# Kernel optimization log

Measured on AMD Instinct MI355X. Metric: run time of the kernel, lower is better.

The kernel has to match this reference:

```python
import jax, jax.numpy as jnp
import numpy as np
from jax import lax

N, C, A, K, D = 2, 256, 3, 20, 256  # batch, channels, anchors, topk person cells, rn_fc_dim
BOX = 4
SIZES = [(80, 128), (40, 64), (20, 32), (10, 16)]
DN = ('NCHW', 'OIHW', 'NCHW')


def _conv(x, w, b):
    return lax.conv_general_dilated(x, w, (1, 1), 'SAME', dimension_numbers=DN) + b[None, :, None, None]


def setup_inputs() -> dict:
    key = jax.random.key(0)
    ks = iter(jax.random.split(key, 40))
    d = {}
    for i, (h, w) in enumerate(SIZES):
        d['feat%d' % i] = jax.random.normal(next(ks), (N, C, h, w), jnp.float32)
    def wfn(shape, s=0.05):
        return jax.random.normal(next(ks), shape, jnp.float32) * s
    d['pc1_w'] = wfn((C, C, 3, 3)); d['pc1_b'] = jnp.zeros((C,), jnp.float32)
    d['pc2_w'] = wfn((C, C, 3, 3)); d['pc2_b'] = jnp.zeros((C,), jnp.float32)
    d['oc1_w'] = wfn((C, C, 3, 3)); d['oc1_b'] = jnp.zeros((C,), jnp.float32)
    d['oc2_w'] = wfn((C, C, 3, 3)); d['oc2_b'] = jnp.zeros((C,), jnp.float32)
    # relation-net FCs: first takes concat(object, person) -> 2C in
    d['rn1_w'] = wfn((D, 2 * C)); d['rn1_b'] = jnp.zeros((D,), jnp.float32)
    d['rn2_w'] = wfn((D, D)); d['rn2_b'] = jnp.zeros((D,), jnp.float32)
    # heads
    d['pl_w'] = wfn((A, C, 1, 1), 0.01); d['pl_b'] = jnp.zeros((A,), jnp.float32)
    d['pd_w'] = wfn((A * BOX, C, 1, 1), 0.01); d['pd_b'] = jnp.zeros((A * BOX,), jnp.float32)
    d['ol_w'] = wfn((A, D), 0.01); d['ol_b'] = jnp.zeros((A,), jnp.float32)
    d['od_w'] = wfn((A * BOX, C, 1, 1), 0.01); d['od_b'] = jnp.zeros((A * BOX,), jnp.float32)
    return d


def _find_top_cells(hidden, logits, topk):
    hid_l, sc_l = [], []
    for h_map, lg in zip(hidden, logits):
        n, c, H, W = h_map.shape
        cell_scores = jnp.max(lg, axis=1).reshape(n, -1)          # (N, HW)
        ts, tc = lax.top_k(cell_scores, topk)                      # (N, K)
        hv = h_map.reshape(n, c, -1)                               # (N, C, HW)
        hid_l.append(jnp.take_along_axis(hv, tc[:, None, :], axis=2))  # (N, C, K)
        sc_l.append(ts)
    scores = jnp.concatenate(sc_l, axis=1)                         # (N, L*K)
    hid = jnp.concatenate(hid_l, axis=2)                           # (N, C, L*K)
    _, keep = lax.top_k(scores, topk)
    return jnp.take_along_axis(hid, keep[:, None, :], axis=2)      # (N, C, K)


def _forward(feats, pc1_w, pc1_b, pc2_w, pc2_b, oc1_w, oc1_b, oc2_w, oc2_b,
             rn1_w, rn1_b, rn2_w, rn2_b, pl_w, pl_b, pd_w, pd_b, ol_w, ol_b, od_w, od_b):
    # person branch
    p_hid, p_log, p_del = [], [], []
    for x in feats:
        x = jax.nn.relu(_conv(x, pc1_w, pc1_b))
        x = jax.nn.relu(_conv(x, pc2_w, pc2_b))
        p_hid.append(x)
        p_log.append(_conv(x, pl_w, pl_b))
        p_del.append(_conv(x, pd_w, pd_b))
    topk_person = _find_top_cells(p_hid, p_log, K)                 # (N, C, K)
    pf = topk_person.transpose(0, 2, 1)                            # (N, K, C)
    # object branch: fc1(concat(o, p)) == o @ Wo.T + p @ Wp.T + b (concat order: object first)
    Wo, Wp = rn1_w[:, :C], rn1_w[:, C:]
    p_proj = jnp.einsum('nkc,dc->nkd', pf, Wp) + rn1_b             # (N, K, D)
    o_log, o_del = [], []
    for x in feats:
        n, _, H, W = x.shape
        y = jax.nn.relu(_conv(x, oc1_w, oc1_b))
        y = jax.nn.relu(_conv(y, oc2_w, oc2_b))
        o_del.append(_conv(y, od_w, od_b))
        yf = y.reshape(n, C, H * W).transpose(0, 2, 1)             # (N, HW, C)
        o_proj = jnp.einsum('nsc,dc->nsd', yf, Wo)                 # (N, HW, D)
        h = jax.nn.relu(o_proj[:, :, None, :] + p_proj[:, None, :, :])  # (N, HW, K, D)
        h = h.sum(axis=2)                                          # (N, HW, D)
        h = jax.nn.relu(jnp.einsum('nsd,ed->nse', h, rn2_w) + rn2_b)
        ol = jnp.einsum('nsd,ad->nsa', h, ol_w) + ol_b             # (N, HW, A)
        o_log.append(ol.transpose(0, 2, 1).reshape(n, A, H, W))
    return tuple(p_log) + tuple(p_del) + tuple(o_log) + tuple(o_del)


def reference(feat0, feat1, feat2, feat3, pc1_w, pc1_b, pc2_w, pc2_b, oc1_w, oc1_b, oc2_w, oc2_b,
              rn1_w, rn1_b, rn2_w, rn2_b, pl_w, pl_b, pd_w, pd_b, ol_w, ol_b, od_w, od_b):
    return _forward([feat0, feat1, feat2, feat3], pc1_w, pc1_b, pc2_w, pc2_b, oc1_w, oc1_b,
                    oc2_w, oc2_b, rn1_w, rn1_b, rn2_w, rn2_b, pl_w, pl_b, pd_w, pd_b,
                    ol_w, ol_b, od_w, od_b)
```

## Files before the change

### kernel.cpp

```cpp
#include <hip/hip_runtime.h>
#include <cstdint>
#include <cstddef>

typedef __bf16 bf16x8 __attribute__((ext_vector_type(8)));
typedef float  f32x16 __attribute__((ext_vector_type(16)));

union U16 { bf16x8 v; uint4 q; };
union U8  { __bf16 h[4]; unsigned long long u; };

__device__ __forceinline__ int lvl256(int bx) {
    return (bx < 40) ? 0 : (bx < 50) ? 1 : (bx < 53) ? 2 : 3;
}
__device__ __forceinline__ int tbase256(int lv) {
    return (lv == 0) ? 0 : (lv == 1) ? 40 : (lv == 2) ? 50 : 53;
}
__device__ __forceinline__ size_t loffE(int lv) {
    return (lv == 0) ? 0 : (lv == 1) ? 5242880 : (lv == 2) ? 6553600 : 6881280;
}
__device__ __forceinline__ size_t plog_off(int lv) {
    return (lv == 0) ? 0 : (lv == 1) ? 61440 : (lv == 2) ? 76800 : 80640;
}
__device__ __forceinline__ size_t pdel_off(int lv) {
    return (lv == 0) ? 81600 : (lv == 1) ? 327360 : (lv == 2) ? 388800 : 404160;
}
__device__ __forceinline__ size_t olog_off(int lv) {
    return (lv == 0) ? 408000 : (lv == 1) ? 469440 : (lv == 2) ? 484800 : 488640;
}
__device__ __forceinline__ size_t odel_off(int lv) {
    return (lv == 0) ? 489600 : (lv == 1) ? 735360 : (lv == 2) ? 796800 : 812160;
}
__device__ __forceinline__ int soff_l(int lv) {
    return (lv == 0) ? 0 : (lv == 1) ? 20480 : (lv == 2) ? 25600 : 26880;
}

__global__ __launch_bounds__(256) void prep_wtap2_k(
    const float* w0, const float* w1, const float* w2, const float* w3,
    __bf16* d0, __bf16* d1, __bf16* d2, __bf16* d3)
{
    int t = blockIdx.x % 9, which = blockIdx.x / 9;
    int co = blockIdx.y, ci = threadIdx.x;
    const float* src = (which == 0) ? w0 : (which == 1) ? w1 : (which == 2) ? w2 : w3;
    __bf16* dst = (which == 0) ? d0 : (which == 1) ? d1 : (which == 2) ? d2 : d3;
    dst[((size_t)(t * 16 + (ci >> 4)) * 256 + co) * 16 + (ci & 15)] =
        (__bf16)src[(size_t)(co * 256 + ci) * 9 + t];
}

__global__ __launch_bounds__(256) void prep_rel_k(
    const float* __restrict__ rn1w, const float* __restrict__ rn2w,
    float* __restrict__ WpT, __bf16* __restrict__ Wo16, __bf16* __restrict__ rn216,
    unsigned* __restrict__ zrow32)
{
    int d = blockIdx.x, c = threadIdx.x;
    WpT[c * 256 + d] = rn1w[(size_t)d * 512 + 256 + c];
    Wo16[((c >> 4) * 256 + d) * 16 + (c & 15)] = (__bf16)rn1w[(size_t)d * 512 + c];
    rn216[((c >> 4) * 256 + d) * 16 + (c & 15)] = (__bf16)rn2w[(size_t)d * 256 + c];
    if (d == 0 && c < 256) zrow32[c] = 0u;
}

__global__ __launch_bounds__(256) void feat2x16_k(
    const float* f0, const float* f1, const float* f2, const float* f3,
    __bf16* __restrict__ x16)
{
    int bx = blockIdx.x, n = blockIdx.y, z = blockIdx.z;
    int lv = lvl256(bx);
    int HW = 10240 >> (2 * lv);
    int p = (bx - tbase256(lv)) * 256 + threadIdx.x;
    if (p >= HW) return;
    const float* f = (lv == 0) ? f0 : (lv == 1) ? f1 : (lv == 2) ? f2 : f3;
    int ch = z >> 1, u = z & 1;
    const float* src = f + (size_t)n * 256 * HW + (size_t)(ch * 16 + u * 8) * HW + p;
    U16 v;
#pragma unroll
    for (int j = 0; j < 8; ++j) v.v[j] = (__bf16)src[(size_t)j * HW];
    *(uint4*)&x16[loffE(lv) + (size_t)n * HW * 256 + (((size_t)ch * HW + p) << 4) + (u << 3)] = v.q;
}

__global__ __launch_bounds__(256) void conv3x3_v3(
    const __bf16* __restrict__ in16,
    const __bf16* __restrict__ wt0, const __bf16* __restrict__ wt1,
    const float* __restrict__ b0p, const float* __restrict__ b1p,
    const __bf16* __restrict__ zrow,
    __bf16* __restrict__ out0, __bf16* __restrict__ out1)
{
    const int tid = threadIdx.x;
    const int zz = blockIdx.z;
    const int n = zz & 1, br = zz >> 1;
    const __bf16* wt = br ? wt1 : wt0;
    const float* bias = br ? b1p : b0p;
    __bf16* outp = br ? out1 : out0;

    const int bx = blockIdx.x;
    const int lv = lvl256(bx);
    const int lg2W = 7 - lv;
    const int W = 1 << lg2W, H = 80 >> lv;
    const int HW = 10240 >> (2 * lv);
    const size_t ioff = loffE(lv) + (size_t)n * HW * 256;
    const __bf16* inb = in16 + ioff;

    const int tile = bx - tbase256(lv);
    const int sp0 = tile << 8;
    const int npix = min(256, HW - sp0);

    const int w = tid >> 6, l64 = tid & 63;
    const int lane = l64 & 31, half = l64 >> 5;
    const int pix0 = (w << 6) + lane, pix1 = pix0 + 32;
    const int cobase = blockIdx.y << 6;

    int boff0[9], boff1[9];
    {
        const int y0 = sp0 >> lg2W;
        const int py0 = pix0 >> lg2W, px0 = pix0 & (W - 1);
        const int py1 = pix1 >> lg2W, px1 = pix1 & (W - 1);
#pragma unroll
        for (int dy = 0; dy < 3; ++dy)
#pragma unroll
            for (int dx = 0; dx < 3; ++dx) {
                int t = dy * 3 + dx;
                int gy0 = y0 + py0 + dy - 1, gx0 = px0 + dx - 1;
                boff0[t] = ((unsigned)gy0 < (unsigned)H && (unsigned)gx0 < (unsigned)W)
                           ? (((gy0 << lg2W) + gx0) * 32 + half * 16) : -1;
                int gy1 = y0 + py1 + dy - 1, gx1 = px1 + dx - 1;
                boff1[t] = ((unsigned)gy1 < (unsigned)H && (unsigned)gx1 < (unsigned)W)
                           ? (((gy1 << lg2W) + gx1) * 32 + half * 16) : -1;
            }
    }
    const __bf16* zp = zrow + (half << 3);

    f32x16 acc00 = {}, acc01 = {}, acc10 = {}, acc11 = {};

    for (int c16 = 0; c16 < 16; ++c16) {
        const char* curB = (const char*)inb + (size_t)c16 * HW * 32;
        const char* curA = (const char*)wt + ((size_t)c16 * 256 + cobase) * 32
                           + lane * 32 + half * 16;
#pragma unroll
        for (int t = 0; t < 9; ++t) {
            const char* ab = curA + (size_t)t * 131072;
            bf16x8 a0 = *(const bf16x8*)ab;
            bf16x8 a1 = *(const bf16x8*)(ab + 1024);
            const __bf16* q0 = (boff0[t] >= 0) ? (const __bf16*)(curB + boff0[t]) : zp;
            const __bf16* q1 = (boff1[t] >= 0) ? (const __bf16*)(curB + boff1[t]) : zp;
            bf16x8 b0 = *(const bf16x8*)q0;
            bf16x8 b1 = *(const bf16x8*)q1;
            acc00 = __builtin_amdgcn_mfma_f32_32x32x16_bf16(a0, b0, acc00, 0, 0, 0);
            acc01 = __builtin_amdgcn_mfma_f32_32x32x16_bf16(a0, b1, acc01, 0, 0, 0);
            acc10 = __builtin_amdgcn_mfma_f32_32x32x16_bf16(a1, b0, acc10, 0, 0, 0);
            acc11 = __builtin_amdgcn_mfma_f32_32x32x16_bf16(a1, b1, acc11, 0, 0, 0);
        }
    }
    const int pixg0 = sp0 + pix0, pixg1 = sp0 + pix1;
    const bool ok0 = (pix0 < npix), ok1 = (pix1 < npix);
#pragma unroll
    for (int b = 0; b < 2; ++b) {
        const f32x16& A0 = b ? acc10 : acc00;
        const f32x16& A1 = b ? acc11 : acc01;
#pragma unroll
        for (int q = 0; q < 4; ++q) {
            int co0 = cobase + b * 32 + q * 8 + half * 4;
            float4 bq = *(const float4*)&bias[co0];
            U8 v0, v1;
            v0.h[0] = (__bf16)fmaxf(A0[q * 4 + 0] + bq.x, 0.f);
            v0.h[1] = (__bf16)fmaxf(A0[q * 4 + 1] + bq.y, 0.f);
            v0.h[2] = (__bf16)fmaxf(A0[q * 4 + 2] + bq.z, 0.f);
            v0.h[3] = (__bf16)fmaxf(A0[q * 4 + 3] + bq.w, 0.f);
            v1.h[0] = (__bf16)fmaxf(A1[q * 4 + 0] + bq.x, 0.f);
            v1.h[1] = (__bf16)fmaxf(A1[q * 4 + 1] + bq.y, 0.f);
            v1.h[2] = (__bf16)fmaxf(A1[q * 4 + 2] + bq.z, 0.f);
            v1.h[3] = (__bf16)fmaxf(A1[q * 4 + 3] + bq.w, 0.f);
            size_t base = ioff + (((size_t)(co0 >> 4) * HW) << 4) + (co0 & 15);
            if (ok0) *(unsigned long long*)&outp[base + ((size_t)pixg0 << 4)] = v0.u;
            if (ok1) *(unsigned long long*)&outp[base + ((size_t)pixg1 << 4)] = v1.u;
        }
    }
}

__global__ __launch_bounds__(256) void p_heads_v2(
    const __bf16* __restrict__ h16, const float* __restrict__ plw,
    const float* __restrict__ plb, const float* __restrict__ pdw,
    const float* __restrict__ pdb, float* __restrict__ out,
    float* __restrict__ scores)
{
    int bx = blockIdx.x, n = blockIdx.y;
    int lv = lvl256(bx);
    int HW = 10240 >> (2 * lv);
    int p = (bx - tbase256(lv)) * 256 + threadIdx.x;
    if (p >= HW) return;
    size_t ioff = loffE(lv) + (size_t)n * HW * 256;
    float acc[15];
#pragma unroll
    for (int a = 0; a < 15; ++a) acc[a] = 0.f;
    for (int ch = 0; ch < 16; ++ch) {
        size_t base = ioff + (((size_t)ch * HW + p) << 4);
        bf16x8 v0 = *(const bf16x8*)&h16[base];
        bf16x8 v1 = *(const bf16x8*)&h16[base + 8];
#pragma unroll
        for (int j = 0; j < 16; ++j) {
            float vv = (j < 8) ? (float)v0[j] : (float)v1[j - 8];
            int c = ch * 16 + j;
#pragma unroll
            for (int a = 0; a < 3; ++a)  acc[a]     = fmaf(plw[a * 256 + c], vv, acc[a]);
#pragma unroll
            for (int a = 0; a < 12; ++a) acc[3 + a] = fmaf(pdw[a * 256 + c], vv, acc[3 + a]);
        }
    }
    float sc = -INFINITY;
#pragma unroll
    for (int a = 0; a < 3; ++a) {
        float lg = acc[a] + plb[a];
        out[plog_off(lv) + ((size_t)n * 3 + a) * HW + p] = lg;
        sc = fmaxf(sc, lg);
    }
    scores[soff_l(lv) + (size_t)n * HW + p] = sc;
#pragma unroll
    for (int a = 0; a < 12; ++a)
        out[pdel_off(lv) + ((size_t)n * 12 + a) * HW + p] = acc[3 + a] + pdb[a];
}

__global__ __launch_bounds__(256) void o_del_v2(
    const __bf16* __restrict__ h16, const float* __restrict__ odw,
    const float* __restrict__ odb, float* __restrict__ out)
{
    int bx = blockIdx.x, n = blockIdx.y;
    int lv = lvl256(bx);
    int HW = 10240 >> (2 * lv);
    int p = (bx - tbase256(lv)) * 256 + threadIdx.x;
    if (p >= HW) return;
    size_t ioff = loffE(lv) + (size_t)n * HW * 256;
    float acc[12];
#pragma unroll
    for (int a = 0; a < 12; ++a) acc[a] = 0.f;
    for (int ch = 0; ch < 16; ++ch) {
        size_t base = ioff + (((size_t)ch * HW + p) << 4);
        bf16x8 v0 = *(const bf16x8*)&h16[base];
        bf16x8 v1 = *(const bf16x8*)&h16[base + 8];
#pragma unroll
        for (int j = 0; j < 16; ++j) {
            float vv = (j < 8) ? (float)v0[j] : (float)v1[j - 8];
            int c = ch * 16 + j;
#pragma unroll
            for (int a = 0; a < 12; ++a) acc[a] = fmaf(odw[a * 256 + c], vv, acc[a]);
        }
    }
#pragma unroll
    for (int a = 0; a < 12; ++a)
        out[odel_off(lv) + ((size_t)n * 12 + a) * HW + p] = acc[a] + odb[a];
}

__global__ __launch_bounds__(256) void topk_level_k(
    const float* __restrict__ scores, float* __restrict__ lv_sc,
    int* __restrict__ lv_ix)
{
    int l = blockIdx.x, n = blockIdx.y;
    int HW = 10240 >> (2 * l);
    int so = soff_l(l);
    __shared__ float sc[10240];
    __shared__ float rv[256];
    __shared__ int   ri[256];
    int tid = threadIdx.x;
    for (int i = tid; i < HW; i += 256) sc[i] = scores[so + (size_t)n * HW + i];
    __syncthreads();
    for (int r = 0; r < 20; ++r) {
        float bv = -INFINITY; int bi = 0x7fffffff;
        for (int i = tid; i < HW; i += 256) {
            float v = sc[i];
            if (v > bv || (v == bv && i < bi)) { bv = v; bi = i; }
        }
        rv[tid] = bv; ri[tid] = bi;
        __syncthreads();
        for (int off = 128; off > 0; off >>= 1) {
            if (tid < off) {
                float v2 = rv[tid + off]; int i2 = ri[tid + off];
                if (v2 > rv[tid] || (v2 == rv[tid] && i2 < ri[tid])) {
                    rv[tid] = v2; ri[tid] = i2;
                }
            }
            __syncthreads();
        }
        if (tid == 0) {
            int idx = (n * 4 + l) * 20 + r;
            lv_sc[idx] = rv[0];
            lv_ix[idx] = ri[0];
            sc[ri[0]] = -INFINITY;
        }
        __syncthreads();
    }
}

__global__ __launch_bounds__(256) void select_gather_v2(
    const float* __restrict__ lv_sc, const int* __restrict__ lv_ix,
    const __bf16* __restrict__ h16, float* __restrict__ pf)
{
    int n = blockIdx.x;
    __shared__ float gsc[80];
    __shared__ int   gcell[80];
    __shared__ int   selL[20], selC[20];
    __shared__ float rv[256];
    __shared__ int   ri[256];
    int tid = threadIdx.x;
    if (tid < 80) {
        gsc[tid] = lv_sc[n * 80 + tid];
        gcell[tid] = lv_ix[n * 80 + tid];
    }
    __syncthreads();
    for (int r = 0; r < 20; ++r) {
        float bv = -INFINITY; int bi = 0x7fffffff;
        if (tid < 80) { bv = gsc[tid]; bi = tid; }
        rv[tid] = bv; ri[tid] = bi;
        __syncthreads();
        for (int off = 128; off > 0; off >>= 1) {
            if (tid < off) {
                float v2 = rv[tid + off]; int i2 = ri[tid + off];
                if (v2 > rv[tid] || (v2 == rv[tid] && i2 < ri[tid])) {
                    rv[tid] = v2; ri[tid] = i2;
                }
            }
            __syncthreads();
        }
        if (tid == 0) {
            int j = ri[0];
            selL[r] = j / 20;
            selC[r] = gcell[j];
            gsc[j] = -INFINITY;
        }
        __syncthreads();
    }
    for (int t = tid; t < 20 * 256; t += 256) {
        int k = t >> 8, c = t & 255;
        int l = selL[k], cell = selC[k];
        int HW = 10240 >> (2 * l);
        pf[((size_t)n * 20 + k) * 256 + c] =
            (float)h16[loffE(l) + (size_t)n * HW * 256 +
                       (((size_t)(c >> 4) * HW + cell) << 4) + (c & 15)];
    }
}

__global__ __launch_bounds__(256) void pproj_k(
    const float* __restrict__ pf, const float* __restrict__ WpT,
    const float* __restrict__ rn1b, float* __restrict__ pp)
{
    int nk = blockIdx.x;
    int t = threadIdx.x;
    __shared__ float f[256];
    f[t] = pf[(size_t)nk * 256 + t];
    __syncthreads();
    float acc = rn1b[t];
    for (int c = 0; c < 256; ++c) acc = fmaf(f[c], WpT[c * 256 + t], acc);
    pp[(size_t)nk * 256 + t] = acc;
}

__global__ __launch_bounds__(256) void orel_k(
    const __bf16* __restrict__ H16o, const __bf16* __restrict__ Wo16,
    const __bf16* __restrict__ rn216, const float* __restrict__ pp,
    const float* __restrict__ rn2b, const float* __restrict__ olw,
    const float* __restrict__ olb, float* __restrict__ out)
{
    __shared__ __bf16 hb[16 * 64 * 24];
    __shared__ __bf16 pp16[5120];
    const int tid = threadIdx.x;
    const int n = blockIdx.y;
    int bx = blockIdx.x;
    int lv = (bx < 160) ? 0 : (bx < 200) ? 1 : (bx < 210) ? 2 : 3;
    int tb = (lv == 0) ? 0 : (lv == 1) ? 160 : (lv == 2) ? 200 : 210;
    int HW = 10240 >> (2 * lv);
    size_t yoff = loffE(lv) + (size_t)n * HW * 256;
    int p0 = (bx - tb) << 6;
    int npix = min(64, HW - p0);

    {
        const float* ps = pp + (size_t)n * 5120;
        for (int i = tid; i < 1280; i += 256) {
            float4 f = *(const float4*)&ps[i * 4];
            U8 v;
            v.h[0] = (__bf16)f.x; v.h[1] = (__bf16)f.y;
            v.h[2] = (__bf16)f.z; v.h[3] = (__bf16)f.w;
            *(unsigned long long*)&pp16[i * 4] = v.u;
        }
    }
    __syncthreads();

    const int w = tid >> 6, l64 = tid & 63;
    const int lane = l64 & 31, half = l64 >> 5;
    const int dbase = w << 6;

    f32x16 acc00 = {}, acc01 = {}, acc10 = {}, acc11 = {};
    for (int c16 = 0; c16 < 16; ++c16) {
        bf16x8 a0 = *(const bf16x8*)&Wo16[(((c16 << 8) + dbase + lane) << 4) + (half << 3)];
        bf16x8 a1 = *(const bf16x8*)&Wo16[(((c16 << 8) + dbase + 32 + lane) << 4) + (half << 3)];
        bf16x8 b0 = *(const bf16x8*)&H16o[yoff + (((size_t)c16 * HW + p0 + lane) << 4) + (half << 3)];
        bf16x8 b1 = *(const bf16x8*)&H16o[yoff + (((size_t)c16 * HW + p0 + 32 + lane) << 4) + (half << 3)];
        acc00 = __builtin_amdgcn_mfma_f32_32x32x16_bf16(a0, b0, acc00, 0, 0, 0);
        acc01 = __builtin_amdgcn_mfma_f32_32x32x16_bf16(a0, b1, acc01, 0, 0, 0);
        acc10 = __builtin_amdgcn_mfma_f32_32x32x16_bf16(a1, b0, acc10, 0, 0, 0);
        acc11 = __builtin_amdgcn_mfma_f32_32x32x16_bf16(a1, b1, acc11, 0, 0, 0);
    }
#pragma unroll
    for (int b = 0; b < 2; ++b) {
        const f32x16& A0 = b ? acc10 : acc00;
        const f32x16& A1 = b ? acc11 : acc01;
#pragma unroll
        for (int q = 0; q < 4; ++q) {
            int d0 = dbase + b * 32 + q * 8 + half * 4;
            float h0[4] = {0.f, 0.f, 0.f, 0.f}, h1[4] = {0.f, 0.f, 0.f, 0.f};
            for (int k = 0; k < 20; ++k) {
                U8 pk;
                pk.u = *(const unsigned long long*)&pp16[k * 256 + d0];
#pragma unroll
                for (int j = 0; j < 4; ++j) {
                    float pkv = (float)pk.h[j];
                    h0[j] += fmaxf(A0[q * 4 + j] + pkv, 0.f);
                    h1[j] += fmaxf(A1[q * 4 + j] + pkv, 0.f);
                }
            }
            U8 v0, v1;
#pragma unroll
            for (int j = 0; j < 4; ++j) { v0.h[j] = (__bf16)h0[j]; v1.h[j] = (__bf16)h1[j]; }
            *(unsigned long long*)&hb[((d0 >> 4) * 64 + lane) * 24 + (d0 & 15)] = v0.u;
            *(unsigned long long*)&hb[((d0 >> 4) * 64 + 32 + lane) * 24 + (d0 & 15)] = v1.u;
        }
    }
    __syncthreads();
    f32x16 e00 = {}, e01 = {}, e10 = {}, e11 = {};
    for (int d16 = 0; d16 < 16; ++d16) {
        bf16x8 a0 = *(const bf16x8*)&rn216[(((d16 << 8) + dbase + lane) << 4) + (half << 3)];
        bf16x8 a1 = *(const bf16x8*)&rn216[(((d16 << 8) + dbase + 32 + lane) << 4) + (half << 3)];
        bf16x8 b0 = *(const bf16x8*)&hb[(d16 * 64 + lane) * 24 + (half << 3)];
        bf16x8 b1 = *(const bf16x8*)&hb[(d16 * 64 + 32 + lane) * 24 + (half << 3)];
        e00 = __builtin_amdgcn_mfma_f32_32x32x16_bf16(a0, b0, e00, 0, 0, 0);
        e01 = __builtin_amdgcn_mfma_f32_32x32x16_bf16(a0, b1, e01, 0, 0, 0);
        e10 = __builtin_amdgcn_mfma_f32_32x32x16_bf16(a1, b0, e10, 0, 0, 0);
        e11 = __builtin_amdgcn_mfma_f32_32x32x16_bf16(a1, b1, e11, 0, 0, 0);
    }
    __syncthreads();
#pragma unroll
    for (int b = 0; b < 2; ++b) {
        const f32x16& A0 = b ? e10 : e00;
        const f32x16& A1 = b ? e11 : e01;
#pragma unroll
        for (int q = 0; q < 4; ++q) {
            int e0 = dbase + b * 32 + q * 8 + half * 4;
            float4 bb = *(const float4*)&rn2b[e0];
            U8 v0, v1;
            v0.h[0] = (__bf16)fmaxf(A0[q * 4 + 0] + bb.x, 0.f);
            v0.h[1] = (__bf16)fmaxf(A0[q * 4 + 1] + bb.y, 0.f);
            v0.h[2] = (__bf16)fmaxf(A0[q * 4 + 2] + bb.z, 0.f);
            v0.h[3] = (__bf16)fmaxf(A0[q * 4 + 3] + bb.w, 0.f);
            v1.h[0] = (__bf16)fmaxf(A1[q * 4 + 0] + bb.x, 0.f);
            v1.h[1] = (__bf16)fmaxf(A1[q * 4 + 1] + bb.y, 0.f);
            v1.h[2] = (__bf16)fmaxf(A1[q * 4 + 2] + bb.z, 0.f);
            v1.h[3] = (__bf16)fmaxf(A1[q * 4 + 3] + bb.w, 0.f);
            *(unsigned long long*)&hb[((e0 >> 4) * 64 + lane) * 24 + (e0 & 15)] = v0.u;
            *(unsigned long long*)&hb[((e0 >> 4) * 64 + 32 + lane) * 24 + (e0 & 15)] = v1.u;
        }
    }
    __syncthreads();
    if (tid < 192) {
        int px = tid / 3, a = tid - px * 3;
        if (px < npix) {
            float s = olb[a];
            for (int e = 0; e < 256; ++e)
                s = fmaf(olw[a * 256 + e], (float)hb[((e >> 4) * 64 + px) * 24 + (e & 15)], s);
            out[olog_off(lv) + ((size_t)n * 3 + a) * HW + p0 + px] = s;
        }
    }
}

extern "C" void kernel_launch(void* const* d_in, const int* in_sizes, int n_in,
                              void* d_out, int out_size, void* d_ws, size_t ws_size,
                              hipStream_t stream)
{
    const float* feat[4] = {(const float*)d_in[0], (const float*)d_in[1],
                            (const float*)d_in[2], (const float*)d_in[3]};
    const float* pc1w = (const float*)d_in[4];  const float* pc1b = (const float*)d_in[5];
    const float* pc2w = (const float*)d_in[6];  const float* pc2b = (const float*)d_in[7];
    const float* oc1w = (const float*)d_in[8];  const float* oc1b = (const float*)d_in[9];
    const float* oc2w = (const float*)d_in[10]; const float* oc2b = (const float*)d_in[11];
    const float* rn1w = (const float*)d_in[12]; const float* rn1b = (const float*)d_in[13];
    const float* rn2w = (const float*)d_in[14]; const float* rn2b = (const float*)d_in[15];
    const float* plw  = (const float*)d_in[16]; const float* plb  = (const float*)d_in[17];
    const float* pdw  = (const float*)d_in[18]; const float* pdb  = (const float*)d_in[19];
    const float* olw  = (const float*)d_in[20]; const float* olb  = (const float*)d_in[21];
    const float* odw  = (const float*)d_in[22]; const float* odb  = (const float*)d_in[23];

    float* ws = (float*)d_ws;
    __bf16* bufA = (__bf16*)(ws);
    __bf16* bufB = (__bf16*)(ws + 3481600);
    __bf16* bufC = (__bf16*)(ws + 6963200);
    __bf16* wt_pc1 = (__bf16*)(ws + 10444800);
    __bf16* wt_pc2 = wt_pc1 + 589824;
    __bf16* wt_oc1 = wt_pc1 + 2 * 589824;
    __bf16* wt_oc2 = wt_pc1 + 3 * 589824;
    __bf16* Wo16  = (__bf16*)(ws + 11624448);
    __bf16* rn216 = (__bf16*)(ws + 11657216);
    float* WpT    = ws + 11689984;
    float* scores = ws + 11755520;
    float* lv_sc  = ws + 11782720;
    int*   lv_ix  = (int*)(ws + 11782880);
    float* pf     = ws + 11783040;
    float* pp     = ws + 11793280;
    __bf16* zrow  = (__bf16*)(ws + 11803520);
    float* out    = (float*)d_out;

    hipLaunchKernelGGL(prep_wtap2_k, dim3(36, 256), dim3(256), 0, stream,
                       pc1w, pc2w, oc1w, oc2w, wt_pc1, wt_pc2, wt_oc1, wt_oc2);
    hipLaunchKernelGGL(prep_rel_k, dim3(256), dim3(256), 0, stream,
                       rn1w, rn2w, WpT, Wo16, rn216, (unsigned*)zrow);
    hipLaunchKernelGGL(feat2x16_k, dim3(54, 2, 32), dim3(256), 0, stream,
                       feat[0], feat[1], feat[2], feat[3], bufA);

    hipLaunchKernelGGL(conv3x3_v3, dim3(54, 4, 4), dim3(256), 0, stream,
                       bufA, wt_pc1, wt_oc1, pc1b, oc1b, zrow, bufB, bufC);
    hipLaunchKernelGGL(conv3x3_v3, dim3(54, 4, 2), dim3(256), 0, stream,
                       bufB, wt_pc2, wt_pc2, pc2b, pc2b, zrow, bufA, bufA);
    hipLaunchKernelGGL(conv3x3_v3, dim3(54, 4, 2), dim3(256), 0, stream,
                       bufC, wt_oc2, wt_oc2, oc2b, oc2b, zrow, bufB, bufB);

    hipLaunchKernelGGL(p_heads_v2, dim3(54, 2), dim3(256), 0, stream,
                       bufA, plw, plb, pdw, pdb, out, scores);
    hipLaunchKernelGGL(topk_level_k, dim3(4, 2), dim3(256), 0, stream,
                       scores, lv_sc, lv_ix);
    hipLaunchKernelGGL(select_gather_v2, dim3(2), dim3(256), 0, stream,
                       lv_sc, lv_ix, bufA, pf);
    hipLaunchKernelGGL(pproj_k, dim3(40), dim3(256), 0, stream, pf, WpT, rn1b, pp);

    hipLaunchKernelGGL(o_del_v2, dim3(54, 2), dim3(256), 0, stream,
                       bufB, odw, odb, out);
    hipLaunchKernelGGL(orel_k, dim3(213, 2), dim3(256), 0, stream,
                       bufB, Wo16, rn216, pp, rn2b, olw, olb, out);
}
```

Before: 621.3 us.

## Fuse prep and head kernels, stage conv weights in LDS via async loads

Merges the three prep kernels into one launch, with wider per-thread work in the weight and feature packing. The conv3x3 kernel now double-buffers each 16-channel weight slice in shared memory using global_load_lds async copies instead of reading weights directly from global memory. The person and object head kernels are merged into one launch. Per-level top-k, selection, gather and the person projection are fused into one two-block kernel. This cuts launch count and global weight traffic, but the fused top-k kernel runs serially on only two blocks, and the conv kernel gains extra LDS use and barriers.

```diff
diff --git a/kernel.cpp b/kernel.cpp
--- a/kernel.cpp
+++ b/kernel.cpp
@@ -8,6 +8,12 @@
 union U16 { bf16x8 v; uint4 q; };
 union U8  { __bf16 h[4]; unsigned long long u; };
 
+typedef __attribute__((address_space(1))) const unsigned char gas_t;
+typedef __attribute__((address_space(3))) unsigned char las_t;
+__device__ __forceinline__ void async16(const void* g, void* l) {
+    __builtin_amdgcn_global_load_lds((gas_t*)g, (las_t*)l, 16, 0, 0);
+}
+
 __device__ __forceinline__ int lvl256(int bx) {
     return (bx < 40) ? 0 : (bx < 50) ? 1 : (bx < 53) ? 2 : 3;
 }
@@ -33,55 +39,66 @@
     return (lv == 0) ? 0 : (lv == 1) ? 20480 : (lv == 2) ? 25600 : 26880;
 }
 
-__global__ __launch_bounds__(256) void prep_wtap2_k(
-    const float* w0, const float* w1, const float* w2, const float* w3,
-    __bf16* d0, __bf16* d1, __bf16* d2, __bf16* d3)
+__global__ __launch_bounds__(256) void prep_all_k(
+    const float* f0, const float* f1, const float* f2, const float* f3,
+    const float* pc1w, const float* pc2w, const float* oc1w, const float* oc2w,
+    const float* __restrict__ rn1w, const float* __restrict__ rn2w,
+    __bf16* __restrict__ wtap, float* __restrict__ WpT,
+    __bf16* __restrict__ Wo16, __bf16* __restrict__ rn216,
+    unsigned* __restrict__ zrow32, __bf16* __restrict__ x16)
 {
-    int t = blockIdx.x % 9, which = blockIdx.x / 9;
-    int co = blockIdx.y, ci = threadIdx.x;
-    const float* src = (which == 0) ? w0 : (which == 1) ? w1 : (which == 2) ? w2 : w3;
-    __bf16* dst = (which == 0) ? d0 : (which == 1) ? d1 : (which == 2) ? d2 : d3;
-    dst[((size_t)(t * 16 + (ci >> 4)) * 256 + co) * 16 + (ci & 15)] =
-        (__bf16)src[(size_t)(co * 256 + ci) * 9 + t];
-}
-
-__global__ __launch_bounds__(256) void prep_rel_k(
-    const float* __restrict__ rn1w, const float* __restrict__ rn2w,
-    float* __restrict__ WpT, __bf16* __restrict__ Wo16, __bf16* __restrict__ rn216,
-    unsigned* __restrict__ zrow32)
-{
-    int d = blockIdx.x, c = threadIdx.x;
-    WpT[c * 256 + d] = rn1w[(size_t)d * 512 + 256 + c];
-    Wo16[((c >> 4) * 256 + d) * 16 + (c & 15)] = (__bf16)rn1w[(size_t)d * 512 + c];
-    rn216[((c >> 4) * 256 + d) * 16 + (c & 15)] = (__bf16)rn2w[(size_t)d * 256 + c];
-    if (d == 0 && c < 256) zrow32[c] = 0u;
-}
-
-__global__ __launch_bounds__(256) void feat2x16_k(
-    const float* f0, const float* f1, const float* f2, const float* f3,
-    __bf16* __restrict__ x16)
-{
-    int bx = blockIdx.x, n = blockIdx.y, z = blockIdx.z;
-    int lv = lvl256(bx);
-    int HW = 10240 >> (2 * lv);
-    int p = (bx - tbase256(lv)) * 256 + threadIdx.x;
-    if (p >= HW) return;
-    const float* f = (lv == 0) ? f0 : (lv == 1) ? f1 : (lv == 2) ? f2 : f3;
-    int ch = z >> 1, u = z & 1;
-    const float* src = f + (size_t)n * 256 * HW + (size_t)(ch * 16 + u * 8) * HW + p;
-    U16 v;
-#pragma unroll
-    for (int j = 0; j < 8; ++j) v.v[j] = (__bf16)src[(size_t)j * HW];
-    *(uint4*)&x16[loffE(lv) + (size_t)n * HW * 256 + (((size_t)ch * HW + p) << 4) + (u << 3)] = v.q;
-}
-
-__global__ __launch_bounds__(256) void conv3x3_v3(
+    int bid = blockIdx.x, tid = threadIdx.x;
+    if (bid < 576) {
+        int which = bid / 144, r = bid - which * 144, t = r >> 4, c16 = r & 15;
+        const float* src = (which == 0) ? pc1w : (which == 1) ? pc2w
+                         : (which == 2) ? oc1w : oc2w;
+        __bf16* dst = wtap + (size_t)which * 589824;
+        int co = tid;
+        U16 a, b;
+#pragma unroll
+        for (int j = 0; j < 8; ++j)
+            a.v[j] = (__bf16)src[(size_t)(co * 256 + c16 * 16 + j) * 9 + t];
+#pragma unroll
+        for (int j = 0; j < 8; ++j)
+            b.v[j] = (__bf16)src[(size_t)(co * 256 + c16 * 16 + 8 + j) * 9 + t];
+        size_t o = ((size_t)((t * 16 + c16) * 256 + co)) << 4;
+        *(uint4*)&dst[o] = a.q;
+        *(uint4*)&dst[o + 8] = b.q;
+    } else if (bid < 832) {
+        int d = bid - 576, c = tid;
+        WpT[c * 256 + d] = rn1w[(size_t)d * 512 + 256 + c];
+        Wo16[((c >> 4) * 256 + d) * 16 + (c & 15)] = (__bf16)rn1w[(size_t)d * 512 + c];
+        rn216[((c >> 4) * 256 + d) * 16 + (c & 15)] = (__bf16)rn2w[(size_t)d * 256 + c];
+        if (d == 0) zrow32[c] = 0u;
+    } else {
+        int u = bid - 832;
+        int bx = u >> 5, rr = u & 31, n = rr >> 4, ch = rr & 15;
+        int lv = lvl256(bx);
+        int HW = 10240 >> (2 * lv);
+        int p = (bx - tbase256(lv)) * 256 + tid;
+        if (p >= HW) return;
+        const float* f = (lv == 0) ? f0 : (lv == 1) ? f1 : (lv == 2) ? f2 : f3;
+        const float* src = f + (size_t)n * 256 * HW + (size_t)ch * 16 * HW + p;
+        U16 a, b;
+#pragma unroll
+        for (int j = 0; j < 8; ++j) a.v[j] = (__bf16)src[(size_t)j * HW];
+#pragma unroll
+        for (int j = 0; j < 8; ++j) b.v[j] = (__bf16)src[(size_t)(8 + j) * HW];
+        size_t o = loffE(lv) + (size_t)n * HW * 256 + (((size_t)ch * HW + p) << 4);
+        *(uint4*)&x16[o] = a.q;
+        *(uint4*)&x16[o + 8] = b.q;
+    }
+}
+
+__global__ __launch_bounds__(256) void conv3x3_v4(
     const __bf16* __restrict__ in16,
     const __bf16* __restrict__ wt0, const __bf16* __restrict__ wt1,
     const float* __restrict__ b0p, const float* __restrict__ b1p,
     const __bf16* __restrict__ zrow,
     __bf16* __restrict__ out0, __bf16* __restrict__ out1)
 {
+    __shared__ __bf16 Asm[2][9216];
+
     const int tid = threadIdx.x;
     const int zz = blockIdx.z;
     const int n = zz & 1, br = zz >> 1;
@@ -126,17 +143,29 @@
     }
     const __bf16* zp = zrow + (half << 3);
 
+    const char* wtb = (const char*)wt + cobase * 32;
+    auto stage = [&](int c16, int buf) {
+        const char* base = wtb + (size_t)c16 * 8192;
+        for (int u = w; u < 18; u += 4) {
+            int t = u >> 1, hk = u & 1;
+            async16(base + (size_t)t * 131072 + hk * 1024 + l64 * 16,
+                    &Asm[buf][u * 512]);
+        }
+    };
+
     f32x16 acc00 = {}, acc01 = {}, acc10 = {}, acc11 = {};
 
+    stage(0, 0);
+    int buf = 0;
     for (int c16 = 0; c16 < 16; ++c16) {
+        __syncthreads();
+        if (c16 < 15) stage(c16 + 1, buf ^ 1);
         const char* curB = (const char*)inb + (size_t)c16 * HW * 32;
-        const char* curA = (const char*)wt + ((size_t)c16 * 256 + cobase) * 32
-                           + lane * 32 + half * 16;
+        const __bf16* Ab = &Asm[buf][0];
 #pragma unroll
         for (int t = 0; t < 9; ++t) {
-            const char* ab = curA + (size_t)t * 131072;
-            bf16x8 a0 = *(const bf16x8*)ab;
-            bf16x8 a1 = *(const bf16x8*)(ab + 1024);
+            bf16x8 a0 = *(const bf16x8*)&Ab[t * 1024 + lane * 16 + half * 8];
+            bf16x8 a1 = *(const bf16x8*)&Ab[t * 1024 + 512 + lane * 16 + half * 8];
             const __bf16* q0 = (boff0[t] >= 0) ? (const __bf16*)(curB + boff0[t]) : zp;
             const __bf16* q1 = (boff1[t] >= 0) ? (const __bf16*)(curB + boff1[t]) : zp;
             bf16x8 b0 = *(const bf16x8*)q0;
@@ -146,6 +175,7 @@
             acc10 = __builtin_amdgcn_mfma_f32_32x32x16_bf16(a1, b0, acc10, 0, 0, 0);
             acc11 = __builtin_amdgcn_mfma_f32_32x32x16_bf16(a1, b1, acc11, 0, 0, 0);
         }
+        buf ^= 1;
     }
     const int pixg0 = sp0 + pix0, pixg1 = sp0 + pix1;
     const bool ok0 = (pix0 < npix), ok1 = (pix1 < npix);
@@ -173,97 +203,117 @@
     }
 }
 
-__global__ __launch_bounds__(256) void p_heads_v2(
-    const __bf16* __restrict__ h16, const float* __restrict__ plw,
-    const float* __restrict__ plb, const float* __restrict__ pdw,
-    const float* __restrict__ pdb, float* __restrict__ out,
-    float* __restrict__ scores)
+__global__ __launch_bounds__(256) void heads_k(
+    const __bf16* __restrict__ h16p, const __bf16* __restrict__ h16o,
+    const float* __restrict__ plw, const float* __restrict__ plb,
+    const float* __restrict__ pdw, const float* __restrict__ pdb,
+    const float* __restrict__ odw, const float* __restrict__ odb,
+    float* __restrict__ out, float* __restrict__ scores)
 {
-    int bx = blockIdx.x, n = blockIdx.y;
+    int bx = blockIdx.x, n = blockIdx.y, br = blockIdx.z;
     int lv = lvl256(bx);
     int HW = 10240 >> (2 * lv);
     int p = (bx - tbase256(lv)) * 256 + threadIdx.x;
     if (p >= HW) return;
     size_t ioff = loffE(lv) + (size_t)n * HW * 256;
-    float acc[15];
-#pragma unroll
-    for (int a = 0; a < 15; ++a) acc[a] = 0.f;
-    for (int ch = 0; ch < 16; ++ch) {
-        size_t base = ioff + (((size_t)ch * HW + p) << 4);
-        bf16x8 v0 = *(const bf16x8*)&h16[base];
-        bf16x8 v1 = *(const bf16x8*)&h16[base + 8];
-#pragma unroll
-        for (int j = 0; j < 16; ++j) {
-            float vv = (j < 8) ? (float)v0[j] : (float)v1[j - 8];
-            int c = ch * 16 + j;
-#pragma unroll
-            for (int a = 0; a < 3; ++a)  acc[a]     = fmaf(plw[a * 256 + c], vv, acc[a]);
-#pragma unroll
-            for (int a = 0; a < 12; ++a) acc[3 + a] = fmaf(pdw[a * 256 + c], vv, acc[3 + a]);
-        }
-    }
-    float sc = -INFINITY;
-#pragma unroll
-    for (int a = 0; a < 3; ++a) {
-        float lg = acc[a] + plb[a];
-        out[plog_off(lv) + ((size_t)n * 3 + a) * HW + p] = lg;
-        sc = fmaxf(sc, lg);
-    }
-    scores[soff_l(lv) + (size_t)n * HW + p] = sc;
-#pragma unroll
-    for (int a = 0; a < 12; ++a)
-        out[pdel_off(lv) + ((size_t)n * 12 + a) * HW + p] = acc[3 + a] + pdb[a];
-}
-
-__global__ __launch_bounds__(256) void o_del_v2(
-    const __bf16* __restrict__ h16, const float* __restrict__ odw,
-    const float* __restrict__ odb, float* __restrict__ out)
+    if (br == 0) {
+        float acc[15];
+#pragma unroll
+        for (int a = 0; a < 15; ++a) acc[a] = 0.f;
+        for (int ch = 0; ch < 16; ++ch) {
+            size_t base = ioff + (((size_t)ch * HW + p) << 4);
+            bf16x8 v0 = *(const bf16x8*)&h16p[base];
+            bf16x8 v1 = *(const bf16x8*)&h16p[base + 8];
+#pragma unroll
+            for (int j = 0; j < 16; ++j) {
+                float vv = (j < 8) ? (float)v0[j] : (float)v1[j - 8];
+                int c = ch * 16 + j;
+#pragma unroll
+                for (int a = 0; a < 3; ++a)  acc[a]     = fmaf(plw[a * 256 + c], vv, acc[a]);
+#pragma unroll
+                for (int a = 0; a < 12; ++a) acc[3 + a] = fmaf(pdw[a * 256 + c], vv, acc[3 + a]);
+            }
+        }
+        float sc = -INFINITY;
+#pragma unroll
+        for (int a = 0; a < 3; ++a) {
+            float lg = acc[a] + plb[a];
+            out[plog_off(lv) + ((size_t)n * 3 + a) * HW + p] = lg;
+            sc = fmaxf(sc, lg);
+        }
+        scores[soff_l(lv) + (size_t)n * HW + p] = sc;
+#pragma unroll
+        for (int a = 0; a < 12; ++a)
+            out[pdel_off(lv) + ((size_t)n * 12 + a) * HW + p] = acc[3 + a] + pdb[a];
+    } else {
+        float acc[12];
+#pragma unroll
+        for (int a = 0; a < 12; ++a) acc[a] = 0.f;
+        for (int ch = 0; ch < 16; ++ch) {
+            size_t base = ioff + (((size_t)ch * HW + p) << 4);
+            bf16x8 v0 = *(const bf16x8*)&h16o[base];
+            bf16x8 v1 = *(const bf16x8*)&h16o[base + 8];
+#pragma unroll
+            for (int j = 0; j < 16; ++j) {
+                float vv = (j < 8) ? (float)v0[j] : (float)v1[j - 8];
+                int c = ch * 16 + j;
+#pragma unroll
+                for (int a = 0; a < 12; ++a) acc[a] = fmaf(odw[a * 256 + c], vv, acc[a]);
+            }
+        }
+#pragma unroll
+        for (int a = 0; a < 12; ++a)
+            out[odel_off(lv) + ((size_t)n * 12 + a) * HW + p] = acc[a] + odb[a];
+    }
+}
+
+__global__ __launch_bounds__(256) void topk_fused_k(
+    const float* __restrict__ scores, const __bf16* __restrict__ h16p,
+    const float* __restrict__ WpT, const float* __restrict__ rn1b,
+    float* __restrict__ pp)
 {
-    int bx = blockIdx.x, n = blockIdx.y;
-    int lv = lvl256(bx);
-    int HW = 10240 >> (2 * lv);
-    int p = (bx - tbase256(lv)) * 256 + threadIdx.x;
-    if (p >= HW) return;
-    size_t ioff = loffE(lv) + (size_t)n * HW * 256;
-    float acc[12];
-#pragma unroll
-    for (int a = 0; a < 12; ++a) acc[a] = 0.f;
-    for (int ch = 0; ch < 16; ++ch) {
-        size_t base = ioff + (((size_t)ch * HW + p) << 4);
-        bf16x8 v0 = *(const bf16x8*)&h16[base];
-        bf16x8 v1 = *(const bf16x8*)&h16[base + 8];
-#pragma unroll
-        for (int j = 0; j < 16; ++j) {
-            float vv = (j < 8) ? (float)v0[j] : (float)v1[j - 8];
-            int c = ch * 16 + j;
-#pragma unroll
-            for (int a = 0; a < 12; ++a) acc[a] = fmaf(odw[a * 256 + c], vv, acc[a]);
-        }
-    }
-#pragma unroll
-    for (int a = 0; a < 12; ++a)
-        out[odel_off(lv) + ((size_t)n * 12 + a) * HW + p] = acc[a] + odb[a];
-}
-
-__global__ __launch_bounds__(256) void topk_level_k(
-    const float* __restrict__ scores, float* __restrict__ lv_sc,
-    int* __restrict__ lv_ix)
-{
-    int l = blockIdx.x, n = blockIdx.y;
-    int HW = 10240 >> (2 * l);
-    int so = soff_l(l);
+    int n = blockIdx.x, tid = threadIdx.x;
     __shared__ float sc[10240];
     __shared__ float rv[256];
     __shared__ int   ri[256];
-    int tid = threadIdx.x;
-    for (int i = tid; i < HW; i += 256) sc[i] = scores[so + (size_t)n * HW + i];
-    __syncthreads();
+    __shared__ float lvv[80];
+    __shared__ int   lvi[80];
+    __shared__ int   selL[20], selC[20];
+    __shared__ float pfL[5120];
+
+    for (int l = 0; l < 4; ++l) {
+        int HW = 10240 >> (2 * l);
+        int so = soff_l(l);
+        for (int i = tid; i < HW; i += 256) sc[i] = scores[so + (size_t)n * HW + i];
+        __syncthreads();
+        for (int r = 0; r < 20; ++r) {
+            float bv = -INFINITY; int bi = 0x7fffffff;
+            for (int i = tid; i < HW; i += 256) {
+                float v = sc[i];
+                if (v > bv || (v == bv && i < bi)) { bv = v; bi = i; }
+            }
+            rv[tid] = bv; ri[tid] = bi;
+            __syncthreads();
+            for (int off = 128; off > 0; off >>= 1) {
+                if (tid < off) {
+                    float v2 = rv[tid + off]; int i2 = ri[tid + off];
+                    if (v2 > rv[tid] || (v2 == rv[tid] && i2 < ri[tid])) {
+                        rv[tid] = v2; ri[tid] = i2;
+                    }
+                }
+                __syncthreads();
+            }
+            if (tid == 0) {
+                lvv[l * 20 + r] = rv[0];
+                lvi[l * 20 + r] = ri[0];
+                sc[ri[0]] = -INFINITY;
+            }
+            __syncthreads();
+        }
+    }
     for (int r = 0; r < 20; ++r) {
         float bv = -INFINITY; int bi = 0x7fffffff;
-        for (int i = tid; i < HW; i += 256) {
-            float v = sc[i];
-            if (v > bv || (v == bv && i < bi)) { bv = v; bi = i; }
-        }
+        if (tid < 80) { bv = lvv[tid]; bi = tid; }
         rv[tid] = bv; ri[tid] = bi;
         __syncthreads();
         for (int off = 128; off > 0; off >>= 1) {
@@ -276,75 +326,34 @@
             __syncthreads();
         }
         if (tid == 0) {
-            int idx = (n * 4 + l) * 20 + r;
-            lv_sc[idx] = rv[0];
-            lv_ix[idx] = ri[0];
-            sc[ri[0]] = -INFINITY;
-        }
-        __syncthreads();
-    }
-}
-
-__global__ __launch_bounds__(256) void select_gather_v2(
-    const float* __restrict__ lv_sc, const int* __restrict__ lv_ix,
-    const __bf16* __restrict__ h16, float* __restrict__ pf)
-{
-    int n = blockIdx.x;
-    __shared__ float gsc[80];
-    __shared__ int   gcell[80];
-    __shared__ int   selL[20], selC[20];
-    __shared__ float rv[256];
-    __shared__ int   ri[256];
-    int tid = threadIdx.x;
-    if (tid < 80) {
-        gsc[tid] = lv_sc[n * 80 + tid];
-        gcell[tid] = lv_ix[n * 80 + tid];
-    }
-    __syncthreads();
-    for (int r = 0; r < 20; ++r) {
-        float bv = -INFINITY; int bi = 0x7fffffff;
-        if (tid < 80) { bv = gsc[tid]; bi = tid; }
-        rv[tid] = bv; ri[tid] = bi;
-        __syncthreads();
-        for (int off = 128; off > 0; off >>= 1) {
-            if (tid < off) {
-                float v2 = rv[tid + off]; int i2 = ri[tid + off];
-                if (v2 > rv[tid] || (v2 == rv[tid] && i2 < ri[tid])) {
-                    rv[tid] = v2; ri[tid] = i2;
-                }
-            }
-            __syncthreads();
-        }
-        if (tid == 0) {
             int j = ri[0];
             selL[r] = j / 20;
-            selC[r] = gcell[j];
-            gsc[j] = -INFINITY;
+            selC[r] = lvi[j];
+            lvv[j] = -INFINITY;
         }
         __syncthreads();
     }
-    for (int t = tid; t < 20 * 256; t += 256) {
+    for (int t = tid; t < 5120; t += 256) {
         int k = t >> 8, c = t & 255;
         int l = selL[k], cell = selC[k];
         int HW = 10240 >> (2 * l);
-        pf[((size_t)n * 20 + k) * 256 + c] =
-            (float)h16[loffE(l) + (size_t)n * HW * 256 +
-                       (((size_t)(c >> 4) * HW + cell) << 4) + (c & 15)];
-    }
-}
-
-__global__ __launch_bounds__(256) void pproj_k(
-    const float* __restrict__ pf, const float* __restrict__ WpT,
-    const float* __restrict__ rn1b, float* __restrict__ pp)
-{
-    int nk = blockIdx.x;
-    int t = threadIdx.x;
-    __shared__ float f[256];
-    f[t] = pf[(size_t)nk * 256 + t];
+        pfL[k * 256 + c] =
+            (float)h16p[loffE(l) + (size_t)n * HW * 256 +
+                        (((size_t)(c >> 4) * HW + cell) << 4) + (c & 15)];
+    }
     __syncthreads();
-    float acc = rn1b[t];
-    for (int c = 0; c < 256; ++c) acc = fmaf(f[c], WpT[c * 256 + t], acc);
-    pp[(size_t)nk * 256 + t] = acc;
+    float acc[20];
+    float bb = rn1b[tid];
+#pragma unroll
+    for (int k = 0; k < 20; ++k) acc[k] = bb;
+    for (int c = 0; c < 256; ++c) {
+        float wv = WpT[c * 256 + tid];
+#pragma unroll
+        for (int k = 0; k < 20; ++k) acc[k] = fmaf(pfL[k * 256 + c], wv, acc[k]);
+    }
+#pragma unroll
+    for (int k = 0; k < 20; ++k)
+        pp[(size_t)n * 5120 + k * 256 + tid] = acc[k];
 }
 
 __global__ __launch_bounds__(256) void orel_k(
@@ -484,45 +493,37 @@
     __bf16* bufA = (__bf16*)(ws);
     __bf16* bufB = (__bf16*)(ws + 3481600);
     __bf16* bufC = (__bf16*)(ws + 6963200);
-    __bf16* wt_pc1 = (__bf16*)(ws + 10444800);
-    __bf16* wt_pc2 = wt_pc1 + 589824;
-    __bf16* wt_oc1 = wt_pc1 + 2 * 589824;
-    __bf16* wt_oc2 = wt_pc1 + 3 * 589824;
+    __bf16* wtap = (__bf16*)(ws + 10444800);
+    __bf16* wt_pc1 = wtap;
+    __bf16* wt_pc2 = wtap + 589824;
+    __bf16* wt_oc1 = wtap + 2 * 589824;
+    __bf16* wt_oc2 = wtap + 3 * 589824;
     __bf16* Wo16  = (__bf16*)(ws + 11624448);
     __bf16* rn216 = (__bf16*)(ws + 11657216);
     float* WpT    = ws + 11689984;
     float* scores = ws + 11755520;
-    float* lv_sc  = ws + 11782720;
-    int*   lv_ix  = (int*)(ws + 11782880);
-    float* pf     = ws + 11783040;
     float* pp     = ws + 11793280;
     __bf16* zrow  = (__bf16*)(ws + 11803520);
     float* out    = (float*)d_out;
 
-    hipLaunchKernelGGL(prep_wtap2_k, dim3(36, 256), dim3(256), 0, stream,
-                       pc1w, pc2w, oc1w, oc2w, wt_pc1, wt_pc2, wt_oc1, wt_oc2);
-    hipLaunchKernelGGL(prep_rel_k, dim3(256), dim3(256), 0, stream,
-                       rn1w, rn2w, WpT, Wo16, rn216, (unsigned*)zrow);
-    hipLaunchKernelGGL(feat2x16_k, dim3(54, 2, 32), dim3(256), 0, stream,
-                       feat[0], feat[1], feat[2], feat[3], bufA);
-
-    hipLaunchKernelGGL(conv3x3_v3, dim3(54, 4, 4), dim3(256), 0, stream,
+    hipLaunchKernelGGL(prep_all_k, dim3(2560), dim3(256), 0, stream,
+                       feat[0], feat[1], feat[2], feat[3],
+                       pc1w, pc2w, oc1w, oc2w, rn1w, rn2w,
+                       wtap, WpT, Wo16, rn216, (unsigned*)zrow, bufA);
+
+    hipLaunchKernelGGL(conv3x3_v4, dim3(54, 4, 4), dim3(256), 0, stream,
                        bufA, wt_pc1, wt_oc1, pc1b, oc1b, zrow, bufB, bufC);
-    hipLaunchKernelGGL(conv3x3_v3, dim3(54, 4, 2), dim3(256), 0, stream,
+    hipLaunchKernelGGL(conv3x3_v4, dim3(54, 4, 2), dim3(256), 0, stream,
                        bufB, wt_pc2, wt_pc2, pc2b, pc2b, zrow, bufA, bufA);
-    hipLaunchKernelGGL(conv3x3_v3, dim3(54, 4, 2), dim3(256), 0, stream,
+    hipLaunchKernelGGL(conv3x3_v4, dim3(54, 4, 2), dim3(256), 0, stream,
                        bufC, wt_oc2, wt_oc2, oc2b, oc2b, zrow, bufB, bufB);
 
-    hipLaunchKernelGGL(p_heads_v2, dim3(54, 2), dim3(256), 0, stream,
-                       bufA, plw, plb, pdw, pdb, out, scores);
-    hipLaunchKernelGGL(topk_level_k, dim3(4, 2), dim3(256), 0, stream,
-                       scores, lv_sc, lv_ix);
-    hipLaunchKernelGGL(select_gather_v2, dim3(2), dim3(256), 0, stream,
-                       lv_sc, lv_ix, bufA, pf);
-    hipLaunchKernelGGL(pproj_k, dim3(40), dim3(256), 0, stream, pf, WpT, rn1b, pp);
-
-    hipLaunchKernelGGL(o_del_v2, dim3(54, 2), dim3(256), 0, stream,
-                       bufB, odw, odb, out);
+    hipLaunchKernelGGL(heads_k, dim3(54, 2, 2), dim3(256), 0, stream,
+                       bufA, bufB, plw, plb, pdw, pdb, odw, odb, out, scores);
+
+    hipLaunchKernelGGL(topk_fused_k, dim3(2), dim3(256), 0, stream,
+                       scores, bufA, WpT, rn1b, pp);
+
     hipLaunchKernelGGL(orel_k, dim3(213, 2), dim3(256), 0, stream,
                        bufB, Wo16, rn216, pp, rn2b, olw, olb, out);
 }
```

New measurement: 661.8 us. 1.07x slower.
